# Optimization experiments

Hardware: AMD Instinct MI355X
Metric: run time of the kernel (lower is better)

## Reference

```python
import jax, jax.numpy as jnp
import numpy as np

# Grid / problem sizes (full-res grid for sp_tensor_1; sp_tensor_2 lives on the half-res grid
# and its indices are multiplied by 2 in forward, so they land on even full-res coords).
B, Z, Y, X = 2, 21, 400, 352
Z2, Y2, X2 = 11, 200, 176
N1, N2 = 160000, 60000
CIN, COUT = 64, 128
EPS = 1e-3  # BatchNorm eps


def _build_rulebook():
    """Precompute the SubMConv3d rulebook (spconv builds this once per indice_key).
    Returns padded gather/scatter index arrays for the 26 non-center taps and N.
    Padding uses index N (a dummy zero row / dropped output row)."""
    rng = np.random.default_rng(0)
    # sp_tensor_2: unique voxels on half-res grid, coords scaled by 2 (as done in forward)
    lin2 = rng.choice(B * Z2 * Y2 * X2, size=N2, replace=False)
    b2 = lin2 // (Z2 * Y2 * X2); r = lin2 % (Z2 * Y2 * X2)
    z2 = r // (Y2 * X2); r = r % (Y2 * X2); y2 = r // X2; x2 = r % X2
    c2 = np.stack([b2, 2 * z2, 2 * y2, 2 * x2], 1).astype(np.int64)
    key2 = ((c2[:, 0] * Z + c2[:, 1]) * Y + c2[:, 2]) * X + c2[:, 3]
    # sp_tensor_1: unique voxels on full-res grid, disjoint from scaled sp2 voxels
    lin1 = rng.choice(B * Z * Y * X, size=N1 + 20000, replace=False)
    lin1 = lin1[~np.isin(lin1, key2)][:N1].astype(np.int64)
    b1 = lin1 // (Z * Y * X); r = lin1 % (Z * Y * X)
    z1 = r // (Y * X); r = r % (Y * X); y1 = r // X; x1 = r % X
    c1 = np.stack([b1, z1, y1, x1], 1)
    coords = np.concatenate([c1, c2], 0)  # [N,4] -- sp1 rows first, matching feature concat
    N = coords.shape[0]
    keys = ((coords[:, 0] * Z + coords[:, 1]) * Y + coords[:, 2]) * X + coords[:, 3]
    order = np.argsort(keys); skeys = keys[order]
    gathers, scatters = [], []
    for dz in (-1, 0, 1):
        for dy in (-1, 0, 1):
            for dx in (-1, 0, 1):
                if dz == 0 and dy == 0 and dx == 0:
                    continue  # center tap handled as a dense identity-indexed GEMM
                q = coords[:, 1:] + np.array([dz, dy, dx])
                valid = (q >= 0).all(1) & (q[:, 0] < Z) & (q[:, 1] < Y) & (q[:, 2] < X)
                qk = ((coords[:, 0] * Z + q[:, 0]) * Y + q[:, 1]) * X + q[:, 2]
                pos = np.clip(np.searchsorted(skeys, qk), 0, N - 1)
                hit = valid & (skeys[pos] == qk)
                gathers.append(order[pos[hit]])
                scatters.append(np.nonzero(hit)[0])
    Pmax = max(len(g) for g in gathers)
    G = np.full((26, Pmax), N, np.int32)
    S = np.full((26, Pmax), N, np.int32)
    for i, (g, s) in enumerate(zip(gathers, scatters)):
        G[i, :len(g)] = g
        S[i, :len(s)] = s
    return G, S, N


def setup_inputs() -> dict:
    G, S, N = _build_rulebook()
    k1, k2, k3, k4 = jax.random.split(jax.random.key(0), 4)
    return {
        "features1": jax.random.normal(k1, (N1, CIN), jnp.float32),
        "features2": jax.random.normal(k2, (N - N1, CIN), jnp.float32),
        "weight": jax.random.normal(k3, (27, CIN, COUT), jnp.float32) * (1.0 / np.sqrt(27 * CIN)),
        "bias": jax.random.normal(k4, (COUT,), jnp.float32) * 0.01,
        "gamma": jnp.ones((COUT,), jnp.float32),
        "beta": jnp.zeros((COUT,), jnp.float32),
        "gather_idx": jnp.asarray(G),
        "scatter_idx": jnp.asarray(S),
    }


def reference(features1, features2, weight, bias, gamma, beta, gather_idx, scatter_idx):
    # forward(): concat features of both sparse tensors along the voxel axis
    feats = jnp.concatenate([features1, features2], axis=0)  # [N, Cin]
    N = feats.shape[0]
    # SubMConv3d via gather-GEMM-scatter over the precomputed rulebook.
    # Center tap (kernel index 13): every output voxel pairs with itself -> dense GEMM.
    out = feats @ weight[13] + bias  # [N, Cout]
    # dummy row N absorbs padded rulebook entries
    out = jnp.concatenate([out, jnp.zeros((1, out.shape[1]), out.dtype)], axis=0)
    feats_pad = jnp.concatenate([feats, jnp.zeros((1, feats.shape[1]), feats.dtype)], axis=0)
    taps = [k for k in range(27) if k != 13]
    for i, k in enumerate(taps):
        msg = feats_pad[gather_idx[i]] @ weight[k]  # [Pmax, Cout]
        out = out.at[scatter_idx[i]].add(msg)
    out = out[:N]
    # BatchNorm1d (training mode: batch statistics, biased variance) + ReLU
    mean = jnp.mean(out, axis=0)
    var = jnp.var(out, axis=0)
    out = (out - mean) * jax.lax.rsqrt(var + EPS) * gamma + beta
    return jax.nn.relu(out)
```

## Files before the change

kernel.cpp:

```cpp
#include <hip/hip_runtime.h>

#define EPS 1e-3f

typedef __attribute__((ext_vector_type(8))) short bf8_t;
typedef __attribute__((ext_vector_type(4))) float f32x4;

static __device__ __forceinline__ unsigned f2bf_pack(float a, float b) {
  union { float f; unsigned u; } ca, cb;
  ca.f = a; cb.f = b;
  unsigned ra = (ca.u + 0x7FFFu + ((ca.u >> 16) & 1u)) >> 16;
  unsigned rb = (cb.u + 0x7FFFu + ((cb.u >> 16) & 1u)) >> 16;
  return ra | (rb << 16);
}
static __device__ __forceinline__ unsigned short f2bf1(float x) {
  union { float f; unsigned u; } c; c.f = x;
  return (unsigned short)((c.u + 0x7FFFu + ((c.u >> 16) & 1u)) >> 16);
}
static __device__ __forceinline__ float bf2f(unsigned bits16) {
  union { unsigned u; float f; } c;
  c.u = bits16 << 16;
  return c.f;
}


__global__ __launch_bounds__(256) void prep(
    const float* __restrict__ W, unsigned short* __restrict__ Wb,
    const float* __restrict__ f1, const float* __restrict__ f2,
    unsigned short* __restrict__ fbuf,
    const int* __restrict__ S, unsigned char* __restrict__ SL,
    int* __restrict__ cnt, int N, int N1, int pm,
    int wblocks, int fblocks, int cpb) {
  const int bid = blockIdx.x;
  if (bid < wblocks) {
    int idx = bid * 256 + threadIdx.x;
    int k = idx & 63, n = (idx >> 6) & 127, t = idx >> 13;
    Wb[idx] = f2bf1(W[((size_t)t * 64 + k) * 128 + n]);
  } else if (bid < wblocks + fblocks) {
    int idx = (bid - wblocks) * 256 + threadIdx.x;
    if (idx >= (N + 1) * 8) return;
    int row = idx >> 3, seg = idx & 7;
    uint4 o = make_uint4(0, 0, 0, 0);
    if (row < N) {
      const float* src = (row < N1) ? (f1 + (size_t)row * 64)
                                    : (f2 + (size_t)(row - N1) * 64);
      float4 v0 = *(const float4*)(src + seg * 8);
      float4 v1 = *(const float4*)(src + seg * 8 + 4);
      o.x = f2bf_pack(v0.x, v0.y); o.y = f2bf_pack(v0.z, v0.w);
      o.z = f2bf_pack(v1.x, v1.y); o.w = f2bf_pack(v1.z, v1.w);
    }
    *(uint4*)(fbuf + (size_t)idx * 8) = o;
  } else {
    int b = bid - wblocks - fblocks;
    int tap = b / cpb;
    int p = (b - tap * cpb) * 256 + threadIdx.x;
    if (p >= pm) return;
    const int idx = tap * pm + p;
    const int s = S[idx];
    if (s < N) SL[idx] = (unsigned char)atomicAdd(&cnt[s], 1);
  }
}

__global__ __launch_bounds__(256) void prefix_base(
    const int* __restrict__ cnt, int2* __restrict__ BC,
    int* __restrict__ gtot, int N) {
  const int t = threadIdx.x;
  const int j0 = blockIdx.x * 1024 + t * 4;
  int c0 = 0, c1 = 0, c2 = 0, c3 = 0;
  if (j0 + 3 < N) {
    int4 c = *(const int4*)(cnt + j0);
    c0 = c.x; c1 = c.y; c2 = c.z; c3 = c.w;
  } else {
    if (j0 < N) c0 = cnt[j0];
    if (j0 + 1 < N) c1 = cnt[j0 + 1];
    if (j0 + 2 < N) c2 = cnt[j0 + 2];
  }
  const int tsum = c0 + c1 + c2 + c3;
  int incl = tsum;
#pragma unroll
  for (int off = 1; off < 64; off <<= 1) {
    int u = __shfl_up(incl, off, 64);
    if ((t & 63) >= off) incl += u;
  }
  __shared__ int wsum[4];
  if ((t & 63) == 63) wsum[t >> 6] = incl;
  __syncthreads();
  if (t == 0) {
    int w0 = wsum[0], w1 = wsum[1], w2 = wsum[2], w3 = wsum[3];
    int gb = atomicAdd(gtot, w0 + w1 + w2 + w3);
    wsum[0] = gb; wsum[1] = gb + w0;
    wsum[2] = gb + w0 + w1; wsum[3] = gb + w0 + w1 + w2;
  }
  __syncthreads();
  const int excl = wsum[t >> 6] + incl - tsum;
  if (j0 < N) BC[j0] = make_int2(excl, c0);
  if (j0 + 1 < N) BC[j0 + 1] = make_int2(excl + c0, c1);
  if (j0 + 2 < N) BC[j0 + 2] = make_int2(excl + c0 + c1, c2);
  if (j0 + 3 < N) BC[j0 + 3] = make_int2(excl + c0 + c1 + c2, c3);
}

__global__ __launch_bounds__(256) void conv_mfma(
    const unsigned short* __restrict__ fbuf,
    const unsigned short* __restrict__ Wb, const float* __restrict__ bias,
    const int* __restrict__ G, const int* __restrict__ S,
    const int2* __restrict__ BC, const unsigned char* __restrict__ SL,
    unsigned short* __restrict__ compact, unsigned short* __restrict__ outb,
    int N, int pm, int cblocks, int cpb) {
  __shared__ unsigned short A[128 * 64];
  __shared__ int g_lds[128];
  __shared__ int d_lds[128];
  const int tid = threadIdx.x;
  const int bid = blockIdx.x;
  const bool is_center = (bid < cblocks);
  const unsigned short* Wt;
  int row0 = 0;

  if (is_center) {
    row0 = bid * 128;
    Wt = Wb + (size_t)13 * 128 * 64;
    if (tid < 128) {
      int g = row0 + tid;
      if (g >= N) g = N;
      g_lds[tid] = g;
    }
  } else {
    const int b = bid - cblocks;
    const int tap = b / cpb;
    const int p0 = (b - tap * cpb) * 128;
    const int* Gi = G + (size_t)tap * pm;
    if (Gi[p0] >= N) return;
    const int ktap = tap + (tap >= 13 ? 1 : 0);
    Wt = Wb + (size_t)ktap * 128 * 64;
    const int* Si = S + (size_t)tap * pm;
    if (tid < 128) {
      int p = p0 + tid;
      int g = N, d = -1;
      if (p < pm) {
        g = Gi[p];
        int s = Si[p];
        if (s < N) d = BC[s].x + (int)SL[(size_t)tap * pm + p];
      }
      g_lds[tid] = g;
      d_lds[tid] = d;
    }
  }
  __syncthreads();

#pragma unroll
  for (int it = 0; it < 4; ++it) {
    int flat = it * 256 + tid;
    int r = flat >> 3, qs = flat & 7;
    int g = g_lds[r];
    uint4 v = *(const uint4*)(fbuf + (size_t)g * 64 + qs * 8);
    int rt = r >> 4, m = r & 15, c = qs >> 2, qq = qs & 3;
    *(uint4*)(A + ((rt * 2 + c) * 64 + qq * 16 + m) * 8) = v;
  }
  __syncthreads();

  const int wave = tid >> 6, lane = tid & 63;
  const int ncol = lane & 15, q2 = lane >> 4;
  bf8_t Bf[2][2];
  float bs[2] = {0.f, 0.f};
#pragma unroll
  for (int ct = 0; ct < 2; ++ct) {
    int col = wave * 32 + ct * 16 + ncol;
    if (is_center) bs[ct] = bias[col];
#pragma unroll
    for (int c = 0; c < 2; ++c)
      Bf[ct][c] = *(const bf8_t*)(Wt + (size_t)col * 64 + c * 32 + q2 * 8);
  }
  f32x4 acc[8][2];
#pragma unroll
  for (int rt = 0; rt < 8; ++rt)
#pragma unroll
    for (int ct = 0; ct < 2; ++ct) acc[rt][ct] = (f32x4){0.f, 0.f, 0.f, 0.f};

#pragma unroll
  for (int rt = 0; rt < 8; ++rt) {
    bf8_t a0 = *(const bf8_t*)(A + ((rt * 2 + 0) * 64 + lane) * 8);
    bf8_t a1 = *(const bf8_t*)(A + ((rt * 2 + 1) * 64 + lane) * 8);
#pragma unroll
    for (int ct = 0; ct < 2; ++ct) {
      acc[rt][ct] = __builtin_amdgcn_mfma_f32_16x16x32_bf16(a0, Bf[ct][0], acc[rt][ct], 0, 0, 0);
      acc[rt][ct] = __builtin_amdgcn_mfma_f32_16x16x32_bf16(a1, Bf[ct][1], acc[rt][ct], 0, 0, 0);
    }
  }

  if (is_center) {
#pragma unroll
    for (int rt = 0; rt < 8; ++rt)
#pragma unroll
      for (int ct = 0; ct < 2; ++ct) {
        int col = wave * 32 + ct * 16 + ncol;
#pragma unroll
        for (int e = 0; e < 4; ++e) {
          int row = row0 + rt * 16 + q2 * 4 + e;
          if (row < N)
            outb[(size_t)row * 128 + col] = f2bf1(acc[rt][ct][e] + bs[ct]);
        }
      }
  } else {
#pragma unroll
    for (int rt = 0; rt < 8; ++rt) {
      int dl[4];
#pragma unroll
      for (int e = 0; e < 4; ++e) dl[e] = d_lds[rt * 16 + q2 * 4 + e];
#pragma unroll
      for (int ct = 0; ct < 2; ++ct) {
        int col = wave * 32 + ct * 16 + ncol;
#pragma unroll
        for (int e = 0; e < 4; ++e)
          if (dl[e] >= 0)
            compact[(size_t)dl[e] * 128 + col] = f2bf1(acc[rt][ct][e]);
      }
    }
  }
}

__global__ __launch_bounds__(256) void combine_c(
    unsigned short* __restrict__ outb, const int2* __restrict__ BC,
    const unsigned short* __restrict__ compact, float* __restrict__ ws,
    int N) {
  const int tid = threadIdx.x;
  const int grp = tid >> 5, l = tid & 31;
  float4 s = make_float4(0.f, 0.f, 0.f, 0.f);
  float4 q = make_float4(0.f, 0.f, 0.f, 0.f);

  for (int j = blockIdx.x * 8 + grp; j < N; j += gridDim.x * 8) {
    int2 bc = BC[j];
    uint2 ov = ((const uint2*)(outb + (size_t)j * 128))[l];
    float4 v;
    v.x = bf2f(ov.x & 0xffffu); v.y = bf2f(ov.x >> 16);
    v.z = bf2f(ov.y & 0xffffu); v.w = bf2f(ov.y >> 16);
    for (int k = 0; k < bc.y; ++k) {
      uint2 mv = ((const uint2*)(compact + (size_t)(bc.x + k) * 128))[l];
      v.x += bf2f(mv.x & 0xffffu); v.y += bf2f(mv.x >> 16);
      v.z += bf2f(mv.y & 0xffffu); v.w += bf2f(mv.y >> 16);
    }
    if (bc.y) {
      uint2 pk;
      pk.x = f2bf_pack(v.x, v.y); pk.y = f2bf_pack(v.z, v.w);
      ((uint2*)(outb + (size_t)j * 128))[l] = pk;
    }
    s.x += v.x; s.y += v.y; s.z += v.z; s.w += v.w;
    q.x += v.x * v.x; q.y += v.y * v.y; q.z += v.z * v.z; q.w += v.w * v.w;
  }

  __shared__ float red[8 * 32 * 9];
  float* my = red + (grp * 32 + l) * 9;
  my[0] = s.x; my[1] = s.y; my[2] = s.z; my[3] = s.w;
  my[4] = q.x; my[5] = q.y; my[6] = q.z; my[7] = q.w;
  __syncthreads();
  {
    int c4 = tid & 31, jj = tid >> 5;
    float v = 0.f;
#pragma unroll
    for (int g = 0; g < 8; ++g) v += red[(g * 32 + c4) * 9 + jj];
    int col = c4 * 4 + (jj & 3);
    unsafeAtomicAdd(&ws[(jj >> 2) * 4096 + col * 16], v);
  }
}

__global__ __launch_bounds__(256) void norm_b(
    const unsigned short* __restrict__ outb, float* __restrict__ out,
    const float* __restrict__ ws, const float* __restrict__ gamma,
    const float* __restrict__ beta, int total8, float invN) {
  const int tid0 = blockIdx.x * 256 + threadIdx.x;
  const int c0 = (tid0 & 15) * 8;
  float sc[8], sh[8];
#pragma unroll
  for (int k = 0; k < 8; ++k) {
    float m = ws[(c0 + k) * 16] * invN;
    float var = ws[4096 + (c0 + k) * 16] * invN - m * m;
    sc[k] = gamma[c0 + k] * rsqrtf(var + EPS);
    sh[k] = beta[c0 + k] - m * sc[k];
  }
  for (int idx = tid0; idx < total8; idx += gridDim.x * 256) {
    uint4 v = *(const uint4*)(outb + (size_t)idx * 8);
    float f0 = bf2f(v.x & 0xffffu), f1 = bf2f(v.x >> 16);
    float f2 = bf2f(v.y & 0xffffu), f3 = bf2f(v.y >> 16);
    float f4 = bf2f(v.z & 0xffffu), f5 = bf2f(v.z >> 16);
    float f6 = bf2f(v.w & 0xffffu), f7 = bf2f(v.w >> 16);
    float4 o0, o1;
    o0.x = fmaxf(f0 * sc[0] + sh[0], 0.f);
    o0.y = fmaxf(f1 * sc[1] + sh[1], 0.f);
    o0.z = fmaxf(f2 * sc[2] + sh[2], 0.f);
    o0.w = fmaxf(f3 * sc[3] + sh[3], 0.f);
    o1.x = fmaxf(f4 * sc[4] + sh[4], 0.f);
    o1.y = fmaxf(f5 * sc[5] + sh[5], 0.f);
    o1.z = fmaxf(f6 * sc[6] + sh[6], 0.f);
    o1.w = fmaxf(f7 * sc[7] + sh[7], 0.f);
    *(float4*)(out + (size_t)idx * 8) = o0;
    *(float4*)(out + (size_t)idx * 8 + 4) = o1;
  }
}


__global__ __launch_bounds__(256) void scatter_R(
    const int* __restrict__ S, int* __restrict__ R, int N, int pm) {
  const int p = blockIdx.x * 256 + threadIdx.x;
  const int i = blockIdx.y;
  if (p >= pm) return;
  const int idx = i * pm + p;
  const int s = S[idx];
  if (s < N) R[(size_t)s * 26 + i] = idx;
}

__global__ __launch_bounds__(256) void center_gemm(
    const float* __restrict__ f1, const float* __restrict__ f2,
    const float* __restrict__ W, const float* __restrict__ bias,
    float* __restrict__ out, int N, int N1) {
  __shared__ float fLDS[128 * 65];
  __shared__ float wLDS[32 * 128];
  const int tid = threadIdx.x;
  const int tx = tid & 15, ty = tid >> 4;
  const int row0 = blockIdx.x * 128;

  for (int k = 0; k < 8; ++k) {
    int flat4 = tid + k * 256;
    int row = flat4 >> 4, c4 = flat4 & 15;
    int grow = row0 + row;
    float4 v = make_float4(0.f, 0.f, 0.f, 0.f);
    if (grow < N) {
      const float* src = (grow < N1) ? (f1 + (size_t)grow * 64)
                                     : (f2 + (size_t)(grow - N1) * 64);
      v = *(const float4*)(src + c4 * 4);
    }
    int l = row * 65 + c4 * 4;
    fLDS[l + 0] = v.x; fLDS[l + 1] = v.y; fLDS[l + 2] = v.z; fLDS[l + 3] = v.w;
  }
  float acc[8][8];
#pragma unroll
  for (int r = 0; r < 8; ++r)
#pragma unroll
    for (int j = 0; j < 8; ++j) acc[r][j] = 0.f;
  for (int kk = 0; kk < 64; kk += 32) {
    __syncthreads();
    for (int k = 0; k < 4; ++k) {
      int flat4 = tid + k * 256;
      int c = flat4 >> 5, col4 = flat4 & 31;
      float4 v = *(const float4*)(W + (size_t)(kk + c) * 128 + col4 * 4);
      *(float4*)(wLDS + c * 128 + col4 * 4) = v;
    }
    __syncthreads();
#pragma unroll 4
    for (int c = 0; c < 32; ++c) {
      float a[8];
#pragma unroll
      for (int r = 0; r < 8; ++r) a[r] = fLDS[(ty * 8 + r) * 65 + kk + c];
      float4 b0 = *(const float4*)(wLDS + c * 128 + tx * 8);
      float4 b1 = *(const float4*)(wLDS + c * 128 + tx * 8 + 4);
      float b[8] = {b0.x, b0.y, b0.z, b0.w, b1.x, b1.y, b1.z, b1.w};
#pragma unroll
      for (int r = 0; r < 8; ++r)
#pragma unroll
        for (int j = 0; j < 8; ++j) acc[r][j] += a[r] * b[j];
    }
  }
  float4 bi0 = *(const float4*)(bias + tx * 8);
  float4 bi1 = *(const float4*)(bias + tx * 8 + 4);
#pragma unroll
  for (int r = 0; r < 8; ++r) {
    int grow = row0 + ty * 8 + r;
    if (grow < N) {
      float4 o0 = make_float4(acc[r][0] + bi0.x, acc[r][1] + bi0.y,
                              acc[r][2] + bi0.z, acc[r][3] + bi0.w);
      float4 o1 = make_float4(acc[r][4] + bi1.x, acc[r][5] + bi1.y,
                              acc[r][6] + bi1.z, acc[r][7] + bi1.w);
      float* dst = out + (size_t)grow * 128 + tx * 8;
      *(float4*)dst = o0;
      *(float4*)(dst + 4) = o1;
    }
  }
}

__global__ __launch_bounds__(256) void msg_gemm_buf(
    const float* __restrict__ f1, const float* __restrict__ f2,
    const float* __restrict__ W27, const int* __restrict__ G,
    const int* __restrict__ S, unsigned short* __restrict__ msgbuf,
    int N, int N1, int pm) {
  const int i = blockIdx.y;
  const int ktap = i + (i >= 13 ? 1 : 0);
  const float* W = W27 + (size_t)ktap * 64 * 128;
  const int* Gi = G + (size_t)i * pm;
  const int* Si = S + (size_t)i * pm;
  const int p0 = blockIdx.x * 128;
  if (Si[p0] >= N) return;
  __shared__ float fLDS[128 * 65];
  __shared__ float wLDS[32 * 128];
  const int tid = threadIdx.x;
  const int tx = tid & 15, ty = tid >> 4;
  for (int k = 0; k < 8; ++k) {
    int flat4 = tid + k * 256;
    int row = flat4 >> 4, c4 = flat4 & 15;
    int p = p0 + row;
    float4 v = make_float4(0.f, 0.f, 0.f, 0.f);
    if (p < pm) {
      int g = Gi[p];
      if (g < N) {
        const float* src = (g < N1) ? (f1 + (size_t)g * 64)
                                    : (f2 + (size_t)(g - N1) * 64);
        v = *(const float4*)(src + c4 * 4);
      }
    }
    int l = row * 65 + c4 * 4;
    fLDS[l + 0] = v.x; fLDS[l + 1] = v.y; fLDS[l + 2] = v.z; fLDS[l + 3] = v.w;
  }
  float acc[8][8];
#pragma unroll
  for (int r = 0; r < 8; ++r)
#pragma unroll
    for (int j = 0; j < 8; ++j) acc[r][j] = 0.f;
  for (int kk = 0; kk < 64; kk += 32) {
    __syncthreads();
    for (int k = 0; k < 4; ++k) {
      int flat4 = tid + k * 256;
      int c = flat4 >> 5, col4 = flat4 & 31;
      float4 v = *(const float4*)(W + (size_t)(kk + c) * 128 + col4 * 4);
      *(float4*)(wLDS + c * 128 + col4 * 4) = v;
    }
    __syncthreads();
#pragma unroll 4
    for (int c = 0; c < 32; ++c) {
      float a[8];
#pragma unroll
      for (int r = 0; r < 8; ++r) a[r] = fLDS[(ty * 8 + r) * 65 + kk + c];
      float4 b0 = *(const float4*)(wLDS + c * 128 + tx * 8);
      float4 b1 = *(const float4*)(wLDS + c * 128 + tx * 8 + 4);
      float b[8] = {b0.x, b0.y, b0.z, b0.w, b1.x, b1.y, b1.z, b1.w};
#pragma unroll
      for (int r = 0; r < 8; ++r)
#pragma unroll
        for (int j = 0; j < 8; ++j) acc[r][j] += a[r] * b[j];
    }
  }
#pragma unroll
  for (int r = 0; r < 8; ++r) {
    int p = p0 + ty * 8 + r;
    if (p < pm) {
      uint4 pk;
      pk.x = f2bf_pack(acc[r][0], acc[r][1]);
      pk.y = f2bf_pack(acc[r][2], acc[r][3]);
      pk.z = f2bf_pack(acc[r][4], acc[r][5]);
      pk.w = f2bf_pack(acc[r][6], acc[r][7]);
      *(uint4*)(msgbuf + ((size_t)i * pm + p) * 128 + tx * 8) = pk;
    }
  }
}

__global__ __launch_bounds__(256) void msg_gemm(
    const float* __restrict__ f1, const float* __restrict__ f2,
    const float* __restrict__ W27, const int* __restrict__ G,
    const int* __restrict__ S, float* __restrict__ out,
    int N, int N1, int pm) {
  const int i = blockIdx.y;
  const int ktap = i + (i >= 13 ? 1 : 0);
  const float* W = W27 + (size_t)ktap * 64 * 128;
  const int* Gi = G + (size_t)i * pm;
  const int* Si = S + (size_t)i * pm;
  const int p0 = blockIdx.x * 128;
  if (Si[p0] >= N) return;
  __shared__ float fLDS[128 * 65];
  __shared__ float wLDS[32 * 128];
  const int tid = threadIdx.x;
  const int tx = tid & 15, ty = tid >> 4;
  for (int k = 0; k < 8; ++k) {
    int flat4 = tid + k * 256;
    int row = flat4 >> 4, c4 = flat4 & 15;
    int p = p0 + row;
    float4 v = make_float4(0.f, 0.f, 0.f, 0.f);
    if (p < pm) {
      int g = Gi[p];
      if (g < N) {
        const float* src = (g < N1) ? (f1 + (size_t)g * 64)
                                    : (f2 + (size_t)(g - N1) * 64);
        v = *(const float4*)(src + c4 * 4);
      }
    }
    int l = row * 65 + c4 * 4;
    fLDS[l + 0] = v.x; fLDS[l + 1] = v.y; fLDS[l + 2] = v.z; fLDS[l + 3] = v.w;
  }
  float acc[8][8];
#pragma unroll
  for (int r = 0; r < 8; ++r)
#pragma unroll
    for (int j = 0; j < 8; ++j) acc[r][j] = 0.f;
  for (int kk = 0; kk < 64; kk += 32) {
    __syncthreads();
    for (int k = 0; k < 4; ++k) {
      int flat4 = tid + k * 256;
      int c = flat4 >> 5, col4 = flat4 & 31;
      float4 v = *(const float4*)(W + (size_t)(kk + c) * 128 + col4 * 4);
      *(float4*)(wLDS + c * 128 + col4 * 4) = v;
    }
    __syncthreads();
#pragma unroll 4
    for (int c = 0; c < 32; ++c) {
      float a[8];
#pragma unroll
      for (int r = 0; r < 8; ++r) a[r] = fLDS[(ty * 8 + r) * 65 + kk + c];
      float4 b0 = *(const float4*)(wLDS + c * 128 + tx * 8);
      float4 b1 = *(const float4*)(wLDS + c * 128 + tx * 8 + 4);
      float b[8] = {b0.x, b0.y, b0.z, b0.w, b1.x, b1.y, b1.z, b1.w};
#pragma unroll
      for (int r = 0; r < 8; ++r)
#pragma unroll
        for (int j = 0; j < 8; ++j) acc[r][j] += a[r] * b[j];
    }
  }
#pragma unroll
  for (int r = 0; r < 8; ++r) {
    int p = p0 + ty * 8 + r;
    if (p < pm) {
      int s = Si[p];
      if (s < N) {
        float* dst = out + (size_t)s * 128 + tx * 8;
#pragma unroll
        for (int j = 0; j < 8; ++j) unsafeAtomicAdd(dst + j, acc[r][j]);
      }
    }
  }
}

__global__ __launch_bounds__(256) void combine_stats(
    float* __restrict__ out, const int* __restrict__ R,
    const unsigned short* __restrict__ msgbuf, float* __restrict__ ws,
    int N) {
  const int tid = threadIdx.x;
  const int grp = tid >> 5, l = tid & 31;
  const int base = tid & 32;
  float4 s = make_float4(0.f, 0.f, 0.f, 0.f);
  float4 q = make_float4(0.f, 0.f, 0.f, 0.f);
  for (int j = blockIdx.x * 8 + grp; j < N; j += gridDim.x * 8) {
    float4 v = ((const float4*)(out + (size_t)j * 128))[l];
    int r = (l < 26) ? R[(size_t)j * 26 + l] : -1;
    unsigned long long bal = __ballot(r >= 0);
    unsigned mym = (unsigned)((bal >> base) & 0x3FFFFFFull);
    const bool any = (mym != 0);
    while (mym) {
      int b = __builtin_ctz(mym);
      mym &= mym - 1;
      int ptr = __shfl(r, base + b, 64);
      uint2 mv = ((const uint2*)(msgbuf + (size_t)ptr * 128))[l];
      v.x += bf2f(mv.x & 0xffffu);
      v.y += bf2f(mv.x >> 16);
      v.z += bf2f(mv.y & 0xffffu);
      v.w += bf2f(mv.y >> 16);
    }
    if (any) ((float4*)(out + (size_t)j * 128))[l] = v;
    s.x += v.x; s.y += v.y; s.z += v.z; s.w += v.w;
    q.x += v.x * v.x; q.y += v.y * v.y; q.z += v.z * v.z; q.w += v.w * v.w;
  }
  __shared__ float red[8 * 32 * 8];
  float* my = red + (grp * 32 + l) * 8;
  my[0] = s.x; my[1] = s.y; my[2] = s.z; my[3] = s.w;
  my[4] = q.x; my[5] = q.y; my[6] = q.z; my[7] = q.w;
  __syncthreads();
  {
    int c4 = tid & 31, j = tid >> 5;
    float v = 0.f;
#pragma unroll
    for (int g = 0; g < 8; ++g) v += red[(g * 32 + c4) * 8 + j];
    int col = c4 * 4 + (j & 3);
    unsafeAtomicAdd(&ws[col + (j >> 2) * 128], v);
  }
}

__global__ __launch_bounds__(256) void stats_kernel(
    const float* __restrict__ out, float* __restrict__ ws, int total4) {
  const int tid = threadIdx.x;
  float4 s = make_float4(0.f, 0.f, 0.f, 0.f);
  float4 q = make_float4(0.f, 0.f, 0.f, 0.f);
  const float4* o4 = (const float4*)out;
  for (int idx = blockIdx.x * 256 + tid; idx < total4; idx += gridDim.x * 256) {
    float4 v = o4[idx];
    s.x += v.x; s.y += v.y; s.z += v.z; s.w += v.w;
    q.x += v.x * v.x; q.y += v.y * v.y; q.z += v.z * v.z; q.w += v.w * v.w;
  }
  __shared__ float red[8 * 32 * 8];
  const int col4 = tid & 31, grpq = tid >> 5;
  float* my = red + (grpq * 32 + col4) * 8;
  my[0] = s.x; my[1] = s.y; my[2] = s.z; my[3] = s.w;
  my[4] = q.x; my[5] = q.y; my[6] = q.z; my[7] = q.w;
  __syncthreads();
  {
    int c4 = tid & 31, j = tid >> 5;
    float v = 0.f;
#pragma unroll
    for (int g = 0; g < 8; ++g) v += red[(g * 32 + c4) * 8 + j];
    int col = c4 * 4 + (j & 3);
    unsafeAtomicAdd(&ws[col + (j >> 2) * 128], v);
  }
}

__global__ __launch_bounds__(256) void norm_kernel(
    float* __restrict__ out, const float* __restrict__ ws,
    const float* __restrict__ gamma, const float* __restrict__ beta,
    int total4, float invN) {
  const int tid = threadIdx.x;
  const int c4 = tid & 31;
  float4 s = ((const float4*)ws)[c4];
  float4 q = ((const float4*)ws)[32 + c4];
  float4 g = ((const float4*)gamma)[c4];
  float4 b = ((const float4*)beta)[c4];
  float m0 = s.x * invN, m1 = s.y * invN, m2 = s.z * invN, m3 = s.w * invN;
  float sc0 = g.x * rsqrtf(q.x * invN - m0 * m0 + EPS);
  float sc1 = g.y * rsqrtf(q.y * invN - m1 * m1 + EPS);
  float sc2 = g.z * rsqrtf(q.z * invN - m2 * m2 + EPS);
  float sc3 = g.w * rsqrtf(q.w * invN - m3 * m3 + EPS);
  float sh0 = b.x - m0 * sc0, sh1 = b.y - m1 * sc1;
  float sh2 = b.z - m2 * sc2, sh3 = b.w - m3 * sc3;
  float4* o4 = (float4*)out;
  for (int idx = blockIdx.x * 256 + tid; idx < total4; idx += gridDim.x * 256) {
    float4 v = o4[idx];
    v.x = fmaxf(v.x * sc0 + sh0, 0.f);
    v.y = fmaxf(v.y * sc1 + sh1, 0.f);
    v.z = fmaxf(v.z * sc2 + sh2, 0.f);
    v.w = fmaxf(v.w * sc3 + sh3, 0.f);
    o4[idx] = v;
  }
}

extern "C" void kernel_launch(void* const* d_in, const int* in_sizes, int n_in,
                              void* d_out, int out_size, void* d_ws, size_t ws_size,
                              hipStream_t stream) {
  const float* f1 = (const float*)d_in[0];
  const float* f2 = (const float*)d_in[1];
  const float* W = (const float*)d_in[2];
  const float* bias = (const float*)d_in[3];
  const float* gamma = (const float*)d_in[4];
  const float* beta = (const float*)d_in[5];
  const int* G = (const int*)d_in[6];
  const int* S = (const int*)d_in[7];
  const int N1 = in_sizes[0] / 64;
  const int N2 = in_sizes[1] / 64;
  const int N = N1 + N2;
  const int pm = in_sizes[6] / 26;
  float* out = (float*)d_out;
  float* ws = (float*)d_ws;

  const size_t AL = 255;
  const size_t offC = 32768;
  const size_t Cb = (size_t)N * 4;
  const size_t offBC = (offC + Cb + AL) & ~AL;
  const size_t BCb = (size_t)N * 8;
  const size_t offSL = (offBC + BCb + AL) & ~AL;
  const size_t SLb = (size_t)26 * pm;
  const size_t offF = (offSL + SLb + AL) & ~AL;
  const size_t Fb = (size_t)(N + 1) * 64 * 2;
  const size_t offW = (offF + Fb + AL) & ~AL;
  const size_t Wbyt = (size_t)27 * 128 * 64 * 2;
  const size_t offM = (offW + Wbyt + AL) & ~AL;
  const size_t Mb = (size_t)26 * pm * 128 * 2;
  const size_t offO = (offM + Mb + AL) & ~AL;
  const size_t Ob = (size_t)N * 128 * 2;
  const bool full = ws_size >= offO + Ob;

  const size_t Rb = (size_t)N * 26 * 4;
  const size_t offR2 = 1024;
  const size_t offM2 = (offR2 + Rb + AL) & ~AL;
  const bool fast2 = ws_size >= offM2 + Mb;

  if (full) {
    int* cnt = (int*)((char*)d_ws + offC);
    int2* BC = (int2*)((char*)d_ws + offBC);
    unsigned char* SLp = (unsigned char*)((char*)d_ws + offSL);
    unsigned short* fbuf = (unsigned short*)((char*)d_ws + offF);
    unsigned short* Wb = (unsigned short*)((char*)d_ws + offW);
    unsigned short* compact = (unsigned short*)((char*)d_ws + offM);
    unsigned short* outb = (unsigned short*)((char*)d_ws + offO);
    int* gtot = (int*)((char*)d_ws + 28672);

    const int wblocks = (27 * 128 * 64) / 256;
    const int fblocks = ((N + 1) * 8 + 255) / 256;
    const int cpb256 = (pm + 255) / 256;
    const int cpb128 = (pm + 127) / 128;
    const int cblocks = (N + 127) / 128;

    (void)hipMemsetAsync(ws, 0, offC + Cb, stream);
    prep<<<wblocks + fblocks + 26 * cpb256, 256, 0, stream>>>(
        W, Wb, f1, f2, fbuf, S, SLp, cnt, N, N1, pm, wblocks, fblocks,
        cpb256);
    prefix_base<<<(N + 1023) / 1024, 256, 0, stream>>>(cnt, BC, gtot, N);
    conv_mfma<<<cblocks + 26 * cpb128, 256, 0, stream>>>(
        fbuf, Wb, bias, G, S, BC, SLp, compact, outb, N, pm,
        cblocks, cpb128);
    combine_c<<<2048, 256, 0, stream>>>(outb, BC, compact, ws, N);
    norm_b<<<2048, 256, 0, stream>>>(outb, out, ws, gamma, beta, N * 16,
                                     1.0f / N);
  } else if (fast2) {
    int* R = (int*)((char*)d_ws + offR2);
    unsigned short* msgbuf = (unsigned short*)((char*)d_ws + offM2);
    (void)hipMemsetAsync(ws, 0, 256 * sizeof(float), stream);
    (void)hipMemsetAsync(R, 0xFF, Rb, stream);
    center_gemm<<<(N + 127) / 128, 256, 0, stream>>>(
        f1, f2, W + (size_t)13 * 64 * 128, bias, out, N, N1);
    scatter_R<<<dim3((pm + 255) / 256, 26), 256, 0, stream>>>(S, R, N, pm);
    msg_gemm_buf<<<dim3((pm + 127) / 128, 26), 256, 0, stream>>>(
        f1, f2, W, G, S, msgbuf, N, N1, pm);
    combine_stats<<<1024, 256, 0, stream>>>(out, R, msgbuf, ws, N);
    norm_kernel<<<2048, 256, 0, stream>>>(out, ws, gamma, beta, N * 32,
                                          1.0f / N);
  } else {
    (void)hipMemsetAsync(ws, 0, 256 * sizeof(float), stream);
    center_gemm<<<(N + 127) / 128, 256, 0, stream>>>(
        f1, f2, W + (size_t)13 * 64 * 128, bias, out, N, N1);
    msg_gemm<<<dim3((pm + 127) / 128, 26), 256, 0, stream>>>(
        f1, f2, W, G, S, out, N, N1, pm);
    stats_kernel<<<1024, 256, 0, stream>>>(out, ws, N * 32);
    norm_kernel<<<2048, 256, 0, stream>>>(out, ws, gamma, beta, N * 32,
                                          1.0f / N);
  }
}
```

Measured before the change: 315.4 us.

## Fuse combine and BatchNorm into one cooperative kernel with a grid sync

The center-tap GEMM now writes its biased output into the compact message buffer as slot 0 of each row's segment, so the separate bf16 output buffer goes away. The prefix sum reserves one extra slot per row for this. Combine, statistics and normalize+ReLU are merged into one cooperative kernel that keeps each row's combined values in registers across a grid-wide sync, which removes the second pass over the data and one launch. The fallback path uses two kernels that read through the compact buffer. Risks are heavy register use for the 27-entry keep array, the cost of the grid barrier, and the cooperative launch needing all 1024 blocks resident at once.

```diff
diff --git a/kernel.cpp b/kernel.cpp
--- a/kernel.cpp
+++ b/kernel.cpp
@@ -1,6 +1,8 @@
 #include <hip/hip_runtime.h>
+#include <hip/hip_cooperative_groups.h>
 
 #define EPS 1e-3f
+#define CROWS 27
 
 typedef __attribute__((ext_vector_type(8))) short bf8_t;
 typedef __attribute__((ext_vector_type(4))) float f32x4;
@@ -68,11 +70,11 @@
   int c0 = 0, c1 = 0, c2 = 0, c3 = 0;
   if (j0 + 3 < N) {
     int4 c = *(const int4*)(cnt + j0);
-    c0 = c.x; c1 = c.y; c2 = c.z; c3 = c.w;
+    c0 = c.x + 1; c1 = c.y + 1; c2 = c.z + 1; c3 = c.w + 1;
   } else {
-    if (j0 < N) c0 = cnt[j0];
-    if (j0 + 1 < N) c1 = cnt[j0 + 1];
-    if (j0 + 2 < N) c2 = cnt[j0 + 2];
+    if (j0 < N) c0 = cnt[j0] + 1;
+    if (j0 + 1 < N) c1 = cnt[j0 + 1] + 1;
+    if (j0 + 2 < N) c2 = cnt[j0 + 2] + 1;
   }
   const int tsum = c0 + c1 + c2 + c3;
   int incl = tsum;
@@ -103,7 +105,7 @@
     const unsigned short* __restrict__ Wb, const float* __restrict__ bias,
     const int* __restrict__ G, const int* __restrict__ S,
     const int2* __restrict__ BC, const unsigned char* __restrict__ SL,
-    unsigned short* __restrict__ compact, unsigned short* __restrict__ outb,
+    unsigned short* __restrict__ compact,
     int N, int pm, int cblocks, int cpb) {
   __shared__ unsigned short A[128 * 64];
   __shared__ int g_lds[128];
@@ -112,15 +114,14 @@
   const int bid = blockIdx.x;
   const bool is_center = (bid < cblocks);
   const unsigned short* Wt;
-  int row0 = 0;
 
   if (is_center) {
-    row0 = bid * 128;
+    int row0 = bid * 128;
     Wt = Wb + (size_t)13 * 128 * 64;
     if (tid < 128) {
-      int g = row0 + tid;
-      if (g >= N) g = N;
-      g_lds[tid] = g;
+      int r = row0 + tid;
+      g_lds[tid] = (r < N) ? r : N;
+      d_lds[tid] = (r < N) ? BC[r].x : -1;
     }
   } else {
     const int b = bid - cblocks;
@@ -137,7 +138,7 @@
       if (p < pm) {
         g = Gi[p];
         int s = Si[p];
-        if (s < N) d = BC[s].x + (int)SL[(size_t)tap * pm + p];
+        if (s < N) d = BC[s].x + 1 + (int)SL[(size_t)tap * pm + p];
       }
       g_lds[tid] = g;
       d_lds[tid] = d;
@@ -185,64 +186,57 @@
     }
   }
 
-  if (is_center) {
-#pragma unroll
-    for (int rt = 0; rt < 8; ++rt)
-#pragma unroll
-      for (int ct = 0; ct < 2; ++ct) {
-        int col = wave * 32 + ct * 16 + ncol;
-#pragma unroll
-        for (int e = 0; e < 4; ++e) {
-          int row = row0 + rt * 16 + q2 * 4 + e;
-          if (row < N)
-            outb[(size_t)row * 128 + col] = f2bf1(acc[rt][ct][e] + bs[ct]);
-        }
-      }
-  } else {
-#pragma unroll
-    for (int rt = 0; rt < 8; ++rt) {
-      int dl[4];
-#pragma unroll
-      for (int e = 0; e < 4; ++e) dl[e] = d_lds[rt * 16 + q2 * 4 + e];
-#pragma unroll
-      for (int ct = 0; ct < 2; ++ct) {
-        int col = wave * 32 + ct * 16 + ncol;
-#pragma unroll
-        for (int e = 0; e < 4; ++e)
-          if (dl[e] >= 0)
-            compact[(size_t)dl[e] * 128 + col] = f2bf1(acc[rt][ct][e]);
-      }
-    }
-  }
-}
-
-__global__ __launch_bounds__(256) void combine_c(
-    unsigned short* __restrict__ outb, const int2* __restrict__ BC,
-    const unsigned short* __restrict__ compact, float* __restrict__ ws,
-    int N) {
+#pragma unroll
+  for (int rt = 0; rt < 8; ++rt) {
+    int dl[4];
+#pragma unroll
+    for (int e = 0; e < 4; ++e) dl[e] = d_lds[rt * 16 + q2 * 4 + e];
+#pragma unroll
+    for (int ct = 0; ct < 2; ++ct) {
+      int col = wave * 32 + ct * 16 + ncol;
+#pragma unroll
+      for (int e = 0; e < 4; ++e)
+        if (dl[e] >= 0)
+          compact[(size_t)dl[e] * 128 + col] = f2bf1(acc[rt][ct][e] + bs[ct]);
+    }
+  }
+}
+
+__global__ __launch_bounds__(256, 4) void fused_fin(
+    const unsigned short* __restrict__ compact, const int2* __restrict__ BC,
+    float* __restrict__ ws, const float* __restrict__ gamma,
+    const float* __restrict__ beta, float* __restrict__ out,
+    int N, float invN) {
   const int tid = threadIdx.x;
   const int grp = tid >> 5, l = tid & 31;
+  const int gid = blockIdx.x * 8 + grp;
+  const int j0 = gid * CROWS;
+
+  uint2 keep[CROWS];
   float4 s = make_float4(0.f, 0.f, 0.f, 0.f);
   float4 q = make_float4(0.f, 0.f, 0.f, 0.f);
 
-  for (int j = blockIdx.x * 8 + grp; j < N; j += gridDim.x * 8) {
-    int2 bc = BC[j];
-    uint2 ov = ((const uint2*)(outb + (size_t)j * 128))[l];
-    float4 v;
-    v.x = bf2f(ov.x & 0xffffu); v.y = bf2f(ov.x >> 16);
-    v.z = bf2f(ov.y & 0xffffu); v.w = bf2f(ov.y >> 16);
-    for (int k = 0; k < bc.y; ++k) {
-      uint2 mv = ((const uint2*)(compact + (size_t)(bc.x + k) * 128))[l];
-      v.x += bf2f(mv.x & 0xffffu); v.y += bf2f(mv.x >> 16);
-      v.z += bf2f(mv.y & 0xffffu); v.w += bf2f(mv.y >> 16);
-    }
-    if (bc.y) {
-      uint2 pk;
-      pk.x = f2bf_pack(v.x, v.y); pk.y = f2bf_pack(v.z, v.w);
-      ((uint2*)(outb + (size_t)j * 128))[l] = pk;
-    }
-    s.x += v.x; s.y += v.y; s.z += v.z; s.w += v.w;
-    q.x += v.x * v.x; q.y += v.y * v.y; q.z += v.z * v.z; q.w += v.w * v.w;
+#pragma unroll
+  for (int i = 0; i < CROWS; ++i) {
+    int j = j0 + i;
+    uint2 kv = make_uint2(0, 0);
+    if (j < N) {
+      int2 bc = BC[j];
+      const unsigned short* base = compact + (size_t)bc.x * 128;
+      uint2 mv = ((const uint2*)base)[l];
+      float4 v;
+      v.x = bf2f(mv.x & 0xffffu); v.y = bf2f(mv.x >> 16);
+      v.z = bf2f(mv.y & 0xffffu); v.w = bf2f(mv.y >> 16);
+      for (int k = 1; k < bc.y; ++k) {
+        uint2 m2 = ((const uint2*)(base + (size_t)k * 128))[l];
+        v.x += bf2f(m2.x & 0xffffu); v.y += bf2f(m2.x >> 16);
+        v.z += bf2f(m2.y & 0xffffu); v.w += bf2f(m2.y >> 16);
+      }
+      kv.x = f2bf_pack(v.x, v.y); kv.y = f2bf_pack(v.z, v.w);
+      s.x += v.x; s.y += v.y; s.z += v.z; s.w += v.w;
+      q.x += v.x * v.x; q.y += v.y * v.y; q.z += v.z * v.z; q.w += v.w * v.w;
+    }
+    keep[i] = kv;
   }
 
   __shared__ float red[8 * 32 * 9];
@@ -258,39 +252,103 @@
     int col = c4 * 4 + (jj & 3);
     unsafeAtomicAdd(&ws[(jj >> 2) * 4096 + col * 16], v);
   }
-}
-
-__global__ __launch_bounds__(256) void norm_b(
-    const unsigned short* __restrict__ outb, float* __restrict__ out,
-    const float* __restrict__ ws, const float* __restrict__ gamma,
-    const float* __restrict__ beta, int total8, float invN) {
-  const int tid0 = blockIdx.x * 256 + threadIdx.x;
-  const int c0 = (tid0 & 15) * 8;
-  float sc[8], sh[8];
-#pragma unroll
-  for (int k = 0; k < 8; ++k) {
-    float m = ws[(c0 + k) * 16] * invN;
-    float var = ws[4096 + (c0 + k) * 16] * invN - m * m;
-    sc[k] = gamma[c0 + k] * rsqrtf(var + EPS);
-    sh[k] = beta[c0 + k] - m * sc[k];
-  }
-  for (int idx = tid0; idx < total8; idx += gridDim.x * 256) {
-    uint4 v = *(const uint4*)(outb + (size_t)idx * 8);
-    float f0 = bf2f(v.x & 0xffffu), f1 = bf2f(v.x >> 16);
-    float f2 = bf2f(v.y & 0xffffu), f3 = bf2f(v.y >> 16);
-    float f4 = bf2f(v.z & 0xffffu), f5 = bf2f(v.z >> 16);
-    float f6 = bf2f(v.w & 0xffffu), f7 = bf2f(v.w >> 16);
-    float4 o0, o1;
-    o0.x = fmaxf(f0 * sc[0] + sh[0], 0.f);
-    o0.y = fmaxf(f1 * sc[1] + sh[1], 0.f);
-    o0.z = fmaxf(f2 * sc[2] + sh[2], 0.f);
-    o0.w = fmaxf(f3 * sc[3] + sh[3], 0.f);
-    o1.x = fmaxf(f4 * sc[4] + sh[4], 0.f);
-    o1.y = fmaxf(f5 * sc[5] + sh[5], 0.f);
-    o1.z = fmaxf(f6 * sc[6] + sh[6], 0.f);
-    o1.w = fmaxf(f7 * sc[7] + sh[7], 0.f);
-    *(float4*)(out + (size_t)idx * 8) = o0;
-    *(float4*)(out + (size_t)idx * 8 + 4) = o1;
+
+  cooperative_groups::this_grid().sync();
+
+  float sc[4], sh[4];
+#pragma unroll
+  for (int k = 0; k < 4; ++k) {
+    int col = l * 4 + k;
+    float m = ws[col * 16] * invN;
+    float var = ws[4096 + col * 16] * invN - m * m;
+    sc[k] = gamma[col] * rsqrtf(var + EPS);
+    sh[k] = beta[col] - m * sc[k];
+  }
+
+#pragma unroll
+  for (int i = 0; i < CROWS; ++i) {
+    int j = j0 + i;
+    if (j < N) {
+      uint2 kv = keep[i];
+      float4 o;
+      o.x = fmaxf(bf2f(kv.x & 0xffffu) * sc[0] + sh[0], 0.f);
+      o.y = fmaxf(bf2f(kv.x >> 16) * sc[1] + sh[1], 0.f);
+      o.z = fmaxf(bf2f(kv.y & 0xffffu) * sc[2] + sh[2], 0.f);
+      o.w = fmaxf(bf2f(kv.y >> 16) * sc[3] + sh[3], 0.f);
+      *(float4*)(out + (size_t)j * 128 + l * 4) = o;
+    }
+  }
+}
+
+__global__ __launch_bounds__(256) void combine_c2(
+    unsigned short* __restrict__ compact, const int2* __restrict__ BC,
+    float* __restrict__ ws, int N) {
+  const int tid = threadIdx.x;
+  const int grp = tid >> 5, l = tid & 31;
+  float4 s = make_float4(0.f, 0.f, 0.f, 0.f);
+  float4 q = make_float4(0.f, 0.f, 0.f, 0.f);
+
+  for (int j = blockIdx.x * 8 + grp; j < N; j += gridDim.x * 8) {
+    int2 bc = BC[j];
+    unsigned short* base = compact + (size_t)bc.x * 128;
+    uint2 ov = ((const uint2*)base)[l];
+    float4 v;
+    v.x = bf2f(ov.x & 0xffffu); v.y = bf2f(ov.x >> 16);
+    v.z = bf2f(ov.y & 0xffffu); v.w = bf2f(ov.y >> 16);
+    for (int k = 1; k < bc.y; ++k) {
+      uint2 mv = ((const uint2*)(base + (size_t)k * 128))[l];
+      v.x += bf2f(mv.x & 0xffffu); v.y += bf2f(mv.x >> 16);
+      v.z += bf2f(mv.y & 0xffffu); v.w += bf2f(mv.y >> 16);
+    }
+    if (bc.y > 1) {
+      uint2 pk;
+      pk.x = f2bf_pack(v.x, v.y); pk.y = f2bf_pack(v.z, v.w);
+      ((uint2*)base)[l] = pk;
+    }
+    s.x += v.x; s.y += v.y; s.z += v.z; s.w += v.w;
+    q.x += v.x * v.x; q.y += v.y * v.y; q.z += v.z * v.z; q.w += v.w * v.w;
+  }
+
+  __shared__ float red[8 * 32 * 9];
+  float* my = red + (grp * 32 + l) * 9;
+  my[0] = s.x; my[1] = s.y; my[2] = s.z; my[3] = s.w;
+  my[4] = q.x; my[5] = q.y; my[6] = q.z; my[7] = q.w;
+  __syncthreads();
+  {
+    int c4 = tid & 31, jj = tid >> 5;
+    float v = 0.f;
+#pragma unroll
+    for (int g = 0; g < 8; ++g) v += red[(g * 32 + c4) * 9 + jj];
+    int col = c4 * 4 + (jj & 3);
+    unsafeAtomicAdd(&ws[(jj >> 2) * 4096 + col * 16], v);
+  }
+}
+
+__global__ __launch_bounds__(256) void norm_c2(
+    const unsigned short* __restrict__ compact, const int2* __restrict__ BC,
+    float* __restrict__ out, const float* __restrict__ ws,
+    const float* __restrict__ gamma, const float* __restrict__ beta,
+    int N, float invN) {
+  const int tid = threadIdx.x;
+  const int grp = tid >> 5, l = tid & 31;
+  float sc[4], sh[4];
+#pragma unroll
+  for (int k = 0; k < 4; ++k) {
+    int col = l * 4 + k;
+    float m = ws[col * 16] * invN;
+    float var = ws[4096 + col * 16] * invN - m * m;
+    sc[k] = gamma[col] * rsqrtf(var + EPS);
+    sh[k] = beta[col] - m * sc[k];
+  }
+  for (int j = blockIdx.x * 8 + grp; j < N; j += gridDim.x * 8) {
+    int b = BC[j].x;
+    uint2 kv = ((const uint2*)(compact + (size_t)b * 128))[l];
+    float4 o;
+    o.x = fmaxf(bf2f(kv.x & 0xffffu) * sc[0] + sh[0], 0.f);
+    o.y = fmaxf(bf2f(kv.x >> 16) * sc[1] + sh[1], 0.f);
+    o.z = fmaxf(bf2f(kv.y & 0xffffu) * sc[2] + sh[2], 0.f);
+    o.w = fmaxf(bf2f(kv.y >> 16) * sc[3] + sh[3], 0.f);
+    *(float4*)(out + (size_t)j * 128 + l * 4) = o;
   }
 }
 
@@ -650,15 +708,14 @@
   const size_t offW = (offF + Fb + AL) & ~AL;
   const size_t Wbyt = (size_t)27 * 128 * 64 * 2;
   const size_t offM = (offW + Wbyt + AL) & ~AL;
-  const size_t Mb = (size_t)26 * pm * 128 * 2;
-  const size_t offO = (offM + Mb + AL) & ~AL;
-  const size_t Ob = (size_t)N * 128 * 2;
-  const bool full = ws_size >= offO + Ob;
+  const size_t Mb = ((size_t)N + (size_t)26 * pm + 1024) * 256;
+  const bool full = ws_size >= offM + Mb;
 
   const size_t Rb = (size_t)N * 26 * 4;
   const size_t offR2 = 1024;
   const size_t offM2 = (offR2 + Rb + AL) & ~AL;
-  const bool fast2 = ws_size >= offM2 + Mb;
+  const size_t Mb2 = (size_t)26 * pm * 128 * 2;
+  const bool fast2 = ws_size >= offM2 + Mb2;
 
   if (full) {
     int* cnt = (int*)((char*)d_ws + offC);
@@ -667,7 +724,6 @@
     unsigned short* fbuf = (unsigned short*)((char*)d_ws + offF);
     unsigned short* Wb = (unsigned short*)((char*)d_ws + offW);
     unsigned short* compact = (unsigned short*)((char*)d_ws + offM);
-    unsigned short* outb = (unsigned short*)((char*)d_ws + offO);
     int* gtot = (int*)((char*)d_ws + 28672);
 
     const int wblocks = (27 * 128 * 64) / 256;
@@ -682,11 +738,28 @@
         cpb256);
     prefix_base<<<(N + 1023) / 1024, 256, 0, stream>>>(cnt, BC, gtot, N);
     conv_mfma<<<cblocks + 26 * cpb128, 256, 0, stream>>>(
-        fbuf, Wb, bias, G, S, BC, SLp, compact, outb, N, pm,
-        cblocks, cpb128);
-    combine_c<<<2048, 256, 0, stream>>>(outb, BC, compact, ws, N);
-    norm_b<<<2048, 256, 0, stream>>>(outb, out, ws, gamma, beta, N * 16,
-                                     1.0f / N);
+        fbuf, Wb, bias, G, S, BC, SLp, compact, N, pm, cblocks, cpb128);
+
+    float invN = 1.0f / N;
+    bool coop_ok = (N <= 8192 * CROWS);
+    if (coop_ok) {
+      const unsigned short* compact_c = compact;
+      const int2* BC_c = BC;
+      const float* gamma_c = gamma;
+      const float* beta_c = beta;
+      int Nv = N;
+      void* params[] = {(void*)&compact_c, (void*)&BC_c, (void*)&ws,
+                        (void*)&gamma_c, (void*)&beta_c, (void*)&out,
+                        (void*)&Nv, (void*)&invN};
+      hipError_t e = hipLaunchCooperativeKernel(
+          (const void*)fused_fin, dim3(1024), dim3(256), params, 0, stream);
+      coop_ok = (e == hipSuccess);
+    }
+    if (!coop_ok) {
+      combine_c2<<<2048, 256, 0, stream>>>(compact, BC, ws, N);
+      norm_c2<<<2048, 256, 0, stream>>>(compact, BC, out, ws, gamma, beta,
+                                        N, invN);
+    }
   } else if (fast2) {
     int* R = (int*)((char*)d_ws + offR2);
     unsigned short* msgbuf = (unsigned short*)((char*)d_ws + offM2);
```

Result: slower. 408.0 us (+29.4%).
